# Performance work log

Hardware: AMD Instinct MI355X
Metric: run time of the kernel (lower is better)

## Reference

```python
import jax, jax.numpy as jnp
import numpy as np

N_NODES = 100000
N_EDGES = 1600000
H, D, DE = 4, 32, 32  # heads, node_out_feats, edge_out_feats
NEG_SLOPE = 0.2


def setup_inputs() -> dict:
    key = jax.random.key(0)
    ks = jax.random.split(key, 10)
    return {
        "node_inputs": jax.random.normal(ks[0], (N_NODES, 128), jnp.float32),
        "edge_inputs": jax.random.normal(ks[1], (N_EDGES, 16), jnp.float32),
        "src": jax.random.randint(ks[2], (N_EDGES,), 0, N_NODES, jnp.int32),
        "dst": jax.random.randint(ks[3], (N_EDGES,), 0, N_NODES, jnp.int32),
        "W_fc": jax.random.normal(ks[4], (128, H * D), jnp.float32) * 0.1,
        "attn_src_p": jax.random.normal(ks[5], (1, H, D), jnp.float32) * 0.1,
        "attn_dst_p": jax.random.normal(ks[6], (1, H, D), jnp.float32) * 0.1,
        "W_edge": jax.random.normal(ks[7], (16, H * DE), jnp.float32) * 0.1,
        "attn_edge_p": jax.random.normal(ks[8], (1, H, DE), jnp.float32) * 0.1,
        "W_res": jax.random.normal(ks[9], (128, H * D), jnp.float32) * 0.1,
        "bias_p": jnp.zeros((H * D,), jnp.float32),
    }


def reference(node_inputs, edge_inputs, src, dst, W_fc, attn_src_p,
              attn_dst_p, W_edge, attn_edge_p, W_res, bias_p):
    N = node_inputs.shape[0]
    # node projection: [N, H, D]
    feat = (node_inputs @ W_fc).reshape(N, H, D)
    # per-node attention logits [N, H]
    a_src = (feat * attn_src_p).sum(-1)
    a_dst = (feat * attn_dst_p).sum(-1)
    # edge-feature attention logits [E, H]
    feat_e = (edge_inputs @ W_edge).reshape(-1, H, DE)
    a_edge = (feat_e * attn_edge_p).sum(-1)
    # per-edge score: u_add_v + edge term, then LeakyReLU
    e = a_src[src] + a_dst[dst] + a_edge                 # [E, H]
    e = jnp.where(e > 0, e, NEG_SLOPE * e)
    # edge softmax grouped by destination node
    emax = jax.lax.stop_gradient(jax.ops.segment_max(e, dst, num_segments=N))
    ex = jnp.exp(e - emax[dst])
    denom = jax.ops.segment_sum(ex, dst, num_segments=N)
    attn = ex / denom[dst]                               # [E, H]
    # weighted scatter-aggregate of source features
    msg = feat[src] * attn[:, :, None]                   # [E, H, D]
    x = jax.ops.segment_sum(msg, dst, num_segments=N)    # [N, H, D]
    # residual + bias
    x = x + (node_inputs @ W_res).reshape(N, H, D)
    x = x + bias_p.reshape(H, D)
    return x
```

## Files before the change

kernel.cpp:

```cpp
#include <hip/hip_runtime.h>
#include <math.h>

#define NNODES_FEAT 128
#define HD 128
#define H 4
#define D 32
#define EDGE_F 16
#define NEG_SLOPE 0.2f

typedef _Float16 f16;
typedef _Float16 f16x2 __attribute__((ext_vector_type(2)));
typedef _Float16 f16x4 __attribute__((ext_vector_type(4)));
typedef _Float16 f16x8 __attribute__((ext_vector_type(8)));
typedef float f32x4 __attribute__((ext_vector_type(4)));

union ExPack { float2 f; f16x4 h; };

__global__ void k_wedge(const float* __restrict__ W_edge,
                        const float* __restrict__ attn_edge,
                        float* __restrict__ w_eh) {
    int t = threadIdx.x;
    int k = t >> 2;
    int h = t & 3;
    float s = 0.f;
    for (int d = 0; d < D; ++d)
        s += W_edge[k * HD + h * D + d] * attn_edge[h * D + d];
    w_eh[k * H + h] = s;
}

__global__ __launch_bounds__(256) void k_wt(const float* __restrict__ Wfc,
                                            const float* __restrict__ Wres,
                                            f16* __restrict__ Wt) {
    int i = blockIdx.x * 256 + threadIdx.x;
    int n = i >> 7, k = i & 127;
    float v = (n < 128) ? Wfc[k * HD + n] : Wres[k * HD + (n - 128)];
    Wt[(size_t)n * 128 + k] = (f16)v;
}

#define LDK 136
__global__ __launch_bounds__(256) void k_gemm_mfma(
    const float* __restrict__ A, const f16* __restrict__ Wt,
    const float* __restrict__ bias, f16* __restrict__ feat16,
    float* __restrict__ out, int N) {
    __shared__ f16 As[64 * LDK];
    __shared__ f16 Bs[128 * LDK];
    int tid = threadIdx.x;
    int wave = tid >> 6, lane = tid & 63;
    int m0 = blockIdx.x * 64;
    int cb = blockIdx.y;

    for (int c = tid; c < 64 * 32; c += 256) {
        int r = c >> 5, cc = (c & 31) * 4;
        int gr = m0 + r;
        float4 v = make_float4(0.f, 0.f, 0.f, 0.f);
        if (gr < N) v = *(const float4*)(A + (size_t)gr * 128 + cc);
        f16x4 h = {(f16)v.x, (f16)v.y, (f16)v.z, (f16)v.w};
        *(f16x4*)(&As[r * LDK + cc]) = h;
    }
    const f16* Wblk = Wt + (size_t)cb * 128 * 128;
    for (int c = tid; c < 128 * 16; c += 256) {
        int r = c >> 4, cc = (c & 15) * 8;
        float4 v = *(const float4*)(Wblk + (size_t)r * 128 + cc);
        *(float4*)(&Bs[r * LDK + cc]) = v;
    }
    __syncthreads();

    int am = lane & 15, aq = lane >> 4;
    f32x4 acc[8];
#pragma unroll
    for (int nt = 0; nt < 8; ++nt) acc[nt] = (f32x4){0.f, 0.f, 0.f, 0.f};

    int arow = wave * 16 + am;
#pragma unroll
    for (int kc = 0; kc < 4; ++kc) {
        f16x8 a = *(const f16x8*)(&As[arow * LDK + kc * 32 + aq * 8]);
#pragma unroll
        for (int nt = 0; nt < 8; ++nt) {
            f16x8 b = *(const f16x8*)(&Bs[(nt * 16 + am) * LDK + kc * 32 + aq * 8]);
            acc[nt] = __builtin_amdgcn_mfma_f32_16x16x32_f16(a, b, acc[nt], 0, 0, 0);
        }
    }

    int orow0 = m0 + wave * 16 + aq * 4;
    if (cb == 0) {
#pragma unroll
        for (int nt = 0; nt < 8; ++nt) {
            int col = nt * 16 + am;
#pragma unroll
            for (int r = 0; r < 4; ++r) {
                int row = orow0 + r;
                if (row < N) feat16[(size_t)row * 128 + col] = (f16)acc[nt][r];
            }
        }
    } else {
#pragma unroll
        for (int nt = 0; nt < 8; ++nt) {
            int col = nt * 16 + am;
            float bv = bias[col];
#pragma unroll
            for (int r = 0; r < 4; ++r) {
                int row = orow0 + r;
                if (row < N) out[(size_t)row * 128 + col] = acc[nt][r] + bv;
            }
        }
    }
}

__global__ __launch_bounds__(256) void k_attn_nodes(
    const f16* __restrict__ feat16, const float* __restrict__ attn_src,
    const float* __restrict__ attn_dst, float* __restrict__ a_src,
    float* __restrict__ a_dst, int N) {
    int g = blockIdx.x * 256 + threadIdx.x;
    int n = g >> 2, h = g & 3;
    if (n >= N) return;
    const f16* f = feat16 + (size_t)n * HD + h * D;
    const float* w1 = attn_src + h * D;
    const float* w2 = attn_dst + h * D;
    float s1 = 0.f, s2 = 0.f;
#pragma unroll
    for (int d = 0; d < D; d += 2) {
        f16x2 fv = *(const f16x2*)(f + d);
        float f0 = (float)fv.x, f1 = (float)fv.y;
        s1 += f0 * w1[d] + f1 * w1[d + 1];
        s2 += f0 * w2[d] + f1 * w2[d + 1];
    }
    a_src[n * H + h] = s1;
    a_dst[n * H + h] = s2;
}

__global__ __launch_bounds__(256) void k_count(const int* __restrict__ dst,
                                               int* __restrict__ deg, int E) {
    int e = blockIdx.x * 256 + threadIdx.x;
    if (e < E) atomicAdd(deg + dst[e], 1);
}

__global__ __launch_bounds__(256) void k_scan_partial(
    const int* __restrict__ deg, int* __restrict__ partial, int N) {
    __shared__ int sdata[256];
    int t = threadIdx.x;
    int base = blockIdx.x * 1024 + t * 4;
    int s = 0;
#pragma unroll
    for (int j = 0; j < 4; ++j) { int i = base + j; if (i < N) s += deg[i]; }
    sdata[t] = s;
    __syncthreads();
    for (int off = 128; off > 0; off >>= 1) {
        if (t < off) sdata[t] += sdata[t + off];
        __syncthreads();
    }
    if (t == 0) partial[blockIdx.x] = sdata[0];
}

__global__ __launch_bounds__(256) void k_scan_top(
    int* __restrict__ partial, int* __restrict__ offs, int nb, int N) {
    __shared__ int sdata[256];
    int t = threadIdx.x;
    int v = (t < nb) ? partial[t] : 0;
    sdata[t] = v;
    __syncthreads();
    for (int off = 1; off < 256; off <<= 1) {
        int add = (t >= off) ? sdata[t - off] : 0;
        __syncthreads();
        sdata[t] += add;
        __syncthreads();
    }
    int excl = (t == 0) ? 0 : sdata[t - 1];
    if (t < nb) partial[t] = excl;
    if (t == nb - 1) offs[N] = sdata[t];
}

__global__ __launch_bounds__(256) void k_scan_final(
    int* __restrict__ deg_offs, const int* __restrict__ partial,
    int* __restrict__ cursor, int N) {
    __shared__ int sdata[256];
    int t = threadIdx.x;
    int base = blockIdx.x * 1024 + t * 4;
    int v[4]; int s = 0;
#pragma unroll
    for (int j = 0; j < 4; ++j) { int i = base + j; v[j] = (i < N) ? deg_offs[i] : 0; s += v[j]; }
    sdata[t] = s;
    __syncthreads();
    for (int off = 1; off < 256; off <<= 1) {
        int add = (t >= off) ? sdata[t - off] : 0;
        __syncthreads();
        sdata[t] += add;
        __syncthreads();
    }
    int excl = partial[blockIdx.x] + ((t == 0) ? 0 : sdata[t - 1]);
#pragma unroll
    for (int j = 0; j < 4; ++j) {
        int i = base + j;
        if (i < N) { deg_offs[i] = excl; cursor[i] = excl; excl += v[j]; }
    }
}

__global__ __launch_bounds__(256) void k_edge_fill(
    const float* __restrict__ edge_inputs, const int* __restrict__ src,
    const int* __restrict__ dst, const float* __restrict__ w_eh,
    const float* __restrict__ a_src, const float* __restrict__ a_dst,
    int* __restrict__ cursor, float4* __restrict__ rec, int E) {
    __shared__ float weh_s[EDGE_F * H];
    if (threadIdx.x < EDGE_F * H) weh_s[threadIdx.x] = w_eh[threadIdx.x];
    __syncthreads();

    int base = blockIdx.x * 512 + threadIdx.x;
#pragma unroll
    for (int j = 0; j < 2; ++j) {
        int e = base + j * 256;
        if (e >= E) continue;

        const float* x = edge_inputs + (long)e * EDGE_F;
        float ae[H] = {0.f, 0.f, 0.f, 0.f};
#pragma unroll
        for (int k = 0; k < EDGE_F; ++k) {
            float xv = x[k];
#pragma unroll
            for (int h = 0; h < H; ++h) ae[h] += xv * weh_s[k * H + h];
        }
        int s = src[e], d = dst[e];
        float4 as = *(const float4*)(a_src + s * H);
        float4 ad = *(const float4*)(a_dst + d * H);
        float ev[H];
        ev[0] = as.x + ad.x + ae[0];
        ev[1] = as.y + ad.y + ae[1];
        ev[2] = as.z + ad.z + ae[2];
        ev[3] = as.w + ad.w + ae[3];
#pragma unroll
        for (int h = 0; h < H; ++h) {
            float t = ev[h];
            t = t > 0.f ? t : NEG_SLOPE * t;
            ev[h] = __expf(t);
        }
        int pos = atomicAdd(cursor + d, 1);
        ExPack p;
        p.h = (f16x4){(f16)ev[0], (f16)ev[1], (f16)ev[2], (f16)ev[3]};
        float4 r;
        r.x = __int_as_float(s);
        r.y = p.f.x;
        r.z = p.f.y;
        r.w = 0.f;
        rec[pos] = r;
    }
}

__global__ __launch_bounds__(256) void k_aggr(
    const f16* __restrict__ feat16, const float4* __restrict__ rec,
    const int* __restrict__ offs, float* __restrict__ out, int N) {
    int wave = threadIdx.x >> 6;
    int lane = threadIdx.x & 63;
    int n = blockIdx.x * 4 + wave;
    if (n >= N) return;
    int beg = offs[n], end = offs[n + 1];
    if (end <= beg) return;
    int h = lane >> 4;
    size_t c0 = (size_t)2 * lane;
    float num0 = 0.f, num1 = 0.f, den = 0.f;
    int i = beg;
    for (; i + 3 < end; i += 4) {
        float4 r0 = rec[i], r1 = rec[i + 1], r2 = rec[i + 2], r3 = rec[i + 3];
        int s0 = __float_as_int(r0.x), s1 = __float_as_int(r1.x);
        int s2 = __float_as_int(r2.x), s3 = __float_as_int(r3.x);
        f16x2 f0 = *(const f16x2*)(feat16 + (size_t)s0 * HD + c0);
        f16x2 f1 = *(const f16x2*)(feat16 + (size_t)s1 * HD + c0);
        f16x2 f2 = *(const f16x2*)(feat16 + (size_t)s2 * HD + c0);
        f16x2 f3 = *(const f16x2*)(feat16 + (size_t)s3 * HD + c0);
        ExPack p0, p1, p2, p3;
        p0.f = make_float2(r0.y, r0.z);
        p1.f = make_float2(r1.y, r1.z);
        p2.f = make_float2(r2.y, r2.z);
        p3.f = make_float2(r3.y, r3.z);
        float e0 = (float)p0.h[h], e1 = (float)p1.h[h];
        float e2 = (float)p2.h[h], e3 = (float)p3.h[h];
        num0 += e0 * (float)f0.x + e1 * (float)f1.x + e2 * (float)f2.x + e3 * (float)f3.x;
        num1 += e0 * (float)f0.y + e1 * (float)f1.y + e2 * (float)f2.y + e3 * (float)f3.y;
        den += e0 + e1 + e2 + e3;
    }
    for (; i < end; ++i) {
        float4 r0 = rec[i];
        int s0 = __float_as_int(r0.x);
        f16x2 f0 = *(const f16x2*)(feat16 + (size_t)s0 * HD + c0);
        ExPack p0;
        p0.f = make_float2(r0.y, r0.z);
        float e0 = (float)p0.h[h];
        num0 += e0 * (float)f0.x;
        num1 += e0 * (float)f0.y;
        den += e0;
    }
    float inv = 1.f / den;
    size_t o = (size_t)n * HD + c0;
    float2 v = *(float2*)(out + o);
    v.x += num0 * inv;
    v.y += num1 * inv;
    *(float2*)(out + o) = v;
}

extern "C" void kernel_launch(void* const* d_in, const int* in_sizes, int n_in,
                              void* d_out, int out_size, void* d_ws, size_t ws_size,
                              hipStream_t stream) {
    const float* node_inputs = (const float*)d_in[0];
    const float* edge_inputs = (const float*)d_in[1];
    const int*   src         = (const int*)d_in[2];
    const int*   dst         = (const int*)d_in[3];
    const float* W_fc        = (const float*)d_in[4];
    const float* attn_src_p  = (const float*)d_in[5];
    const float* attn_dst_p  = (const float*)d_in[6];
    const float* W_edge      = (const float*)d_in[7];
    const float* attn_edge_p = (const float*)d_in[8];
    const float* W_res       = (const float*)d_in[9];
    const float* bias_p      = (const float*)d_in[10];

    int N = in_sizes[0] / NNODES_FEAT;
    int E = in_sizes[2];

    float* out = (float*)d_out;

    f16*    feat16  = (f16*)d_ws;
    float4* rec     = (float4*)(feat16 + (size_t)N * HD);
    f16*    Wt      = (f16*)(rec + (size_t)E);
    float*  a_src   = (float*)(Wt + 256 * 128);
    float*  a_dst   = a_src + (size_t)N * H;
    float*  w_eh    = a_dst + (size_t)N * H;
    int*    deg     = (int*)(w_eh + 64);
    int*    offs    = deg;
    int*    cursor  = deg + (N + 2);
    int*    partial = cursor + N;

    hipMemsetAsync(deg, 0, (size_t)(N + 2) * sizeof(int), stream);

    k_wedge<<<1, 64, 0, stream>>>(W_edge, attn_edge_p, w_eh);
    k_wt<<<(256 * 128) / 256, 256, 0, stream>>>(W_fc, W_res, Wt);

    dim3 g1((N + 63) / 64, 2);
    k_gemm_mfma<<<g1, 256, 0, stream>>>(node_inputs, Wt, bias_p, feat16, out, N);

    int nb = (N * H + 255) / 256;
    k_attn_nodes<<<nb, 256, 0, stream>>>(feat16, attn_src_p, attn_dst_p, a_src, a_dst, N);

    int eb = (E + 255) / 256;
    k_count<<<eb, 256, 0, stream>>>(dst, deg, E);
    int sb = (N + 1023) / 1024;
    k_scan_partial<<<sb, 256, 0, stream>>>(deg, partial, N);
    k_scan_top<<<1, 256, 0, stream>>>(partial, offs, sb, N);
    k_scan_final<<<sb, 256, 0, stream>>>(deg, partial, cursor, N);

    int eb2 = (E + 511) / 512;
    k_edge_fill<<<eb2, 256, 0, stream>>>(edge_inputs, src, dst, w_eh, a_src, a_dst,
                                         cursor, rec, E);

    int ab = (N + 3) / 4;
    k_aggr<<<ab, 256, 0, stream>>>(feat16, rec, offs, out, N);
}
```

Measured before the change: 515.4 us.

## Record per-edge rank during counting to remove cursor atomics in edge fill

The counting pass now stores the return value of its atomicAdd as a per-edge rank. The fill kernel then computes each edge's CSR slot as offs[dst] + rank with no second round of atomics, and the separate cursor array goes away. The fill kernel also handles four edges per thread, batches its gather loads up front and reads edge features as float4. This trades a second set of contended atomics for an extra E-sized int array that is written once and read once.

Result: faster. 504.9 us (-2.0%).

```diff
diff --git a/kernel.cpp b/kernel.cpp
--- a/kernel.cpp
+++ b/kernel.cpp
@@ -129,9 +129,14 @@
 }
 
 __global__ __launch_bounds__(256) void k_count(const int* __restrict__ dst,
-                                               int* __restrict__ deg, int E) {
-    int e = blockIdx.x * 256 + threadIdx.x;
-    if (e < E) atomicAdd(deg + dst[e], 1);
+                                               int* __restrict__ deg,
+                                               int* __restrict__ rank, int E) {
+    int base = blockIdx.x * 1024 + threadIdx.x;
+#pragma unroll
+    for (int j = 0; j < 4; ++j) {
+        int e = base + j * 256;
+        if (e < E) rank[e] = atomicAdd(deg + dst[e], 1);
+    }
 }
 
 __global__ __launch_bounds__(256) void k_scan_partial(
@@ -170,8 +175,7 @@
 }
 
 __global__ __launch_bounds__(256) void k_scan_final(
-    int* __restrict__ deg_offs, const int* __restrict__ partial,
-    int* __restrict__ cursor, int N) {
+    int* __restrict__ deg_offs, const int* __restrict__ partial, int N) {
     __shared__ int sdata[256];
     int t = threadIdx.x;
     int base = blockIdx.x * 1024 + t * 4;
@@ -190,7 +194,7 @@
 #pragma unroll
     for (int j = 0; j < 4; ++j) {
         int i = base + j;
-        if (i < N) { deg_offs[i] = excl; cursor[i] = excl; excl += v[j]; }
+        if (i < N) { deg_offs[i] = excl; excl += v[j]; }
     }
 }
 
@@ -198,48 +202,73 @@
     const float* __restrict__ edge_inputs, const int* __restrict__ src,
     const int* __restrict__ dst, const float* __restrict__ w_eh,
     const float* __restrict__ a_src, const float* __restrict__ a_dst,
-    int* __restrict__ cursor, float4* __restrict__ rec, int E) {
+    const int* __restrict__ offs, const int* __restrict__ rank,
+    float4* __restrict__ rec, int E) {
     __shared__ float weh_s[EDGE_F * H];
     if (threadIdx.x < EDGE_F * H) weh_s[threadIdx.x] = w_eh[threadIdx.x];
     __syncthreads();
 
-    int base = blockIdx.x * 512 + threadIdx.x;
-#pragma unroll
-    for (int j = 0; j < 2; ++j) {
+    int base = blockIdx.x * 1024 + threadIdx.x;
+
+    int sj[4], dj[4], rj[4];
+    bool valid[4];
+#pragma unroll
+    for (int j = 0; j < 4; ++j) {
         int e = base + j * 256;
-        if (e >= E) continue;
-
-        const float* x = edge_inputs + (long)e * EDGE_F;
-        float ae[H] = {0.f, 0.f, 0.f, 0.f};
+        valid[j] = (e < E);
+        sj[j] = valid[j] ? src[e] : 0;
+        dj[j] = valid[j] ? dst[e] : 0;
+        rj[j] = valid[j] ? rank[e] : 0;
+    }
+
+    float4 as[4], ad[4];
+    int pos[4];
+#pragma unroll
+    for (int j = 0; j < 4; ++j) {
+        as[j] = *(const float4*)(a_src + sj[j] * H);
+        ad[j] = *(const float4*)(a_dst + dj[j] * H);
+        pos[j] = offs[dj[j]] + rj[j];
+    }
+
+#pragma unroll
+    for (int j = 0; j < 4; ++j) {
+        if (!valid[j]) continue;
+        int e = base + j * 256;
+        const float* x = edge_inputs + (size_t)e * EDGE_F;
+        float4 x0 = *(const float4*)(x);
+        float4 x1 = *(const float4*)(x + 4);
+        float4 x2 = *(const float4*)(x + 8);
+        float4 x3 = *(const float4*)(x + 12);
+        float xs[16] = {x0.x, x0.y, x0.z, x0.w, x1.x, x1.y, x1.z, x1.w,
+                        x2.x, x2.y, x2.z, x2.w, x3.x, x3.y, x3.z, x3.w};
+        float ae0 = 0.f, ae1 = 0.f, ae2 = 0.f, ae3 = 0.f;
 #pragma unroll
         for (int k = 0; k < EDGE_F; ++k) {
-            float xv = x[k];
-#pragma unroll
-            for (int h = 0; h < H; ++h) ae[h] += xv * weh_s[k * H + h];
-        }
-        int s = src[e], d = dst[e];
-        float4 as = *(const float4*)(a_src + s * H);
-        float4 ad = *(const float4*)(a_dst + d * H);
+            float xv = xs[k];
+            ae0 += xv * weh_s[k * H + 0];
+            ae1 += xv * weh_s[k * H + 1];
+            ae2 += xv * weh_s[k * H + 2];
+            ae3 += xv * weh_s[k * H + 3];
+        }
         float ev[H];
-        ev[0] = as.x + ad.x + ae[0];
-        ev[1] = as.y + ad.y + ae[1];
-        ev[2] = as.z + ad.z + ae[2];
-        ev[3] = as.w + ad.w + ae[3];
+        ev[0] = as[j].x + ad[j].x + ae0;
+        ev[1] = as[j].y + ad[j].y + ae1;
+        ev[2] = as[j].z + ad[j].z + ae2;
+        ev[3] = as[j].w + ad[j].w + ae3;
 #pragma unroll
         for (int h = 0; h < H; ++h) {
             float t = ev[h];
             t = t > 0.f ? t : NEG_SLOPE * t;
             ev[h] = __expf(t);
         }
-        int pos = atomicAdd(cursor + d, 1);
         ExPack p;
         p.h = (f16x4){(f16)ev[0], (f16)ev[1], (f16)ev[2], (f16)ev[3]};
         float4 r;
-        r.x = __int_as_float(s);
+        r.x = __int_as_float(sj[j]);
         r.y = p.f.x;
         r.z = p.f.y;
         r.w = 0.f;
-        rec[pos] = r;
+        rec[pos[j]] = r;
     }
 }
 
@@ -322,8 +351,8 @@
     float*  w_eh    = a_dst + (size_t)N * H;
     int*    deg     = (int*)(w_eh + 64);
     int*    offs    = deg;
-    int*    cursor  = deg + (N + 2);
-    int*    partial = cursor + N;
+    int*    partial = deg + (N + 2);
+    int*    rank    = partial + 128;
 
     hipMemsetAsync(deg, 0, (size_t)(N + 2) * sizeof(int), stream);
 
@@ -336,16 +365,15 @@
     int nb = (N * H + 255) / 256;
     k_attn_nodes<<<nb, 256, 0, stream>>>(feat16, attn_src_p, attn_dst_p, a_src, a_dst, N);
 
-    int eb = (E + 255) / 256;
-    k_count<<<eb, 256, 0, stream>>>(dst, deg, E);
+    int eb = (E + 1023) / 1024;
+    k_count<<<eb, 256, 0, stream>>>(dst, deg, rank, E);
     int sb = (N + 1023) / 1024;
     k_scan_partial<<<sb, 256, 0, stream>>>(deg, partial, N);
     k_scan_top<<<1, 256, 0, stream>>>(partial, offs, sb, N);
-    k_scan_final<<<sb, 256, 0, stream>>>(deg, partial, cursor, N);
-
-    int eb2 = (E + 511) / 512;
-    k_edge_fill<<<eb2, 256, 0, stream>>>(edge_inputs, src, dst, w_eh, a_src, a_dst,
-                                         cursor, rec, E);
+    k_scan_final<<<sb, 256, 0, stream>>>(deg, partial, N);
+
+    k_edge_fill<<<eb, 256, 0, stream>>>(edge_inputs, src, dst, w_eh, a_src, a_dst,
+                                        offs, rank, rec, E);
 
     int ab = (N + 3) / 4;
     k_aggr<<<ab, 256, 0, stream>>>(feat16, rec, offs, out, N);
```
